# Optimization experiments

Hardware: AMD Instinct MI355X
Metric: run time of the kernel (lower is better)

Reference implementation:

```python
import jax, jax.numpy as jnp
import numpy as np
import math

N_HEAD = 16
D_MODEL = 1024
KSIZE = 3
PAD = 1


def _conv1d(x, w, b, pad):
    # x: [B, C_in, S], w: [C_out, C_in, K] (torch Conv1d layout)
    y = jax.lax.conv_general_dilated(
        x, w, window_strides=(1,), padding=[(pad, pad)],
        dimension_numbers=("NCH", "OIH", "NCH"))
    return y + b[None, :, None]


def setup_inputs() -> dict:
    key = jax.random.key(0)
    ks = jax.random.split(key, 10)
    B, S, D = 2, 2048, D_MODEL
    sc = 1.0 / math.sqrt(D)
    return {
        "q": jax.random.normal(ks[0], (B, S, D), jnp.float32),
        "k": jax.random.normal(ks[1], (B, S, D), jnp.float32),
        "v": jax.random.normal(ks[2], (B, S, D), jnp.float32),
        "wq_w": jax.random.normal(ks[3], (D, D, KSIZE), jnp.float32) * sc,
        "wq_b": jnp.zeros((D,), jnp.float32),
        "wk_w": jax.random.normal(ks[4], (D, D, KSIZE), jnp.float32) * sc,
        "wk_b": jnp.zeros((D,), jnp.float32),
        "wv_w": jax.random.normal(ks[5], (D, D, 1), jnp.float32) * sc,
        "wv_b": jnp.zeros((D,), jnp.float32),
        "wc_w": jax.random.normal(ks[6], (D, D), jnp.float32) * sc,
        "wc_b": jnp.zeros((D,), jnp.float32),
    }


def reference(q, k, v, wq_w, wq_b, wk_w, wk_b, wv_w, wv_b, wc_w, wc_b):
    B, S, D = q.shape
    h = N_HEAD
    d = D // h
    # channels-first for conv projections: [B, D, S]
    qc = _conv1d(jnp.swapaxes(q, 1, 2), wq_w, wq_b, PAD)
    kc = _conv1d(jnp.swapaxes(k, 1, 2), wk_w, wk_b, PAD)
    vc = _conv1d(jnp.swapaxes(v, 1, 2), wv_w, wv_b, 0)
    # faithful to torch: view(b, d, h, s) then transpose(1,2).transpose(2,3) -> [b, h, s, d]
    # (head index is the FAST axis of the channel dim, matching the original)
    qh = jnp.transpose(qc.reshape(B, d, h, S), (0, 2, 3, 1))
    kh = jnp.transpose(kc.reshape(B, d, h, S), (0, 2, 3, 1))
    vh = jnp.transpose(vc.reshape(B, d, h, S), (0, 2, 3, 1))
    scores = jnp.einsum("bhqd,bhkd->bhqk", qh, kh) / math.sqrt(d)
    attn = jax.nn.softmax(scores, axis=-1)
    out = jnp.einsum("bhqk,bhkd->bhqd", attn, vh)
    # concat: [b,h,s,d] -> [b,s,h*d]
    out = jnp.transpose(out, (0, 2, 1, 3)).reshape(B, S, D)
    # torch Linear: x @ W^T + b
    return out @ wc_w.T + wc_b
```

## Files before the change

kernel.cpp:

```cpp
#include <hip/hip_runtime.h>
#include <hip/hip_bf16.h>

#define SS 2048
#define DDIM 1024

typedef unsigned short u16;
typedef unsigned int u32;
typedef __attribute__((ext_vector_type(8))) short bf16x8_t;
typedef __attribute__((ext_vector_type(4))) float f32x4_t;

__device__ __forceinline__ u16 f2bf(float f) {
  __hip_bfloat16 h = __float2bfloat16(f);
  return *reinterpret_cast<u16*>(&h);
}

__device__ __forceinline__ void gld16(const void* g, void* lds_base) {
  __builtin_amdgcn_global_load_lds(
      (const __attribute__((address_space(1))) u32*)(uintptr_t)g,
      (__attribute__((address_space(3))) u32*)(u32)(uintptr_t)lds_base,
      16, 0, 0);
}

__global__ __launch_bounds__(256) void prep_kernel(
    const float* __restrict__ q, const float* __restrict__ k,
    const float* __restrict__ v, const float* __restrict__ wq_w,
    const float* __restrict__ wk_w, const float* __restrict__ wv_w,
    const float* __restrict__ wc_w, u16* __restrict__ Xq,
    u16* __restrict__ Xk, u16* __restrict__ Xv, u16* __restrict__ Wqr,
    u16* __restrict__ Wkr, u16* __restrict__ Wvr, u16* __restrict__ Wcr,
    u32* __restrict__ zbuf) {
  const int bid = blockIdx.x;
  const int tid = threadIdx.x;
  if (bid == 0 && tid < 64) zbuf[tid] = 0u;

  if (bid < 6144) {
    const int z = bid >> 11;
    const int bx = bid & 2047;
    const float* src = (z == 0) ? q : (z == 1) ? k : v;
    u16* dst = (z == 0) ? Xq : (z == 1) ? Xk : Xv;
    int i = bx * 256 + tid;
    const float4* s = (const float4*)src + (size_t)i * 2;
    float4 f0 = s[0], f1 = s[1];
    u16 o[8] = {f2bf(f0.x), f2bf(f0.y), f2bf(f0.z), f2bf(f0.w),
                f2bf(f1.x), f2bf(f1.y), f2bf(f1.z), f2bf(f1.w)};
    *(uint4*)(dst + (size_t)i * 8) = *(const uint4*)o;
  } else if (bid < 8192) {
    const int idx = bid - 6144;
    const float* w = (idx >= 1024) ? wk_w : wq_w;
    u16* out = (idx >= 1024) ? Wkr : Wqr;
    const int o = idx & 1023;
    for (int j = tid; j < 3072; j += 256) {
      int i = j / 3, t = j - i * 3;
      out[(size_t)o * 3072 + t * 1024 + i] = f2bf(w[(size_t)o * 3072 + j]);
    }
  } else {
    const int idx = bid - 8192;
    const float* w = (idx >= 1024) ? wc_w : wv_w;
    u16* out = (idx >= 1024) ? Wcr : Wvr;
    const int bx = idx & 1023;
    size_t i = (size_t)bx * 1024 + tid * 4;
    float4 f = *(const float4*)(w + i);
    u16 o4[4] = {f2bf(f.x), f2bf(f.y), f2bf(f.z), f2bf(f.w)};
    *(ushort4*)(out + i) = *(const ushort4*)o4;
  }
}

__global__ __launch_bounds__(256) void mfma_proj(
    const u16* __restrict__ Xq, const u16* __restrict__ Xk,
    const u16* __restrict__ Xv, const u16* __restrict__ Wq,
    const u16* __restrict__ Wk, const u16* __restrict__ Wv,
    const float* __restrict__ bq, const float* __restrict__ bk,
    const float* __restrict__ bv, u16* __restrict__ Qhb,
    u16* __restrict__ Khb, u16* __restrict__ Vtb,
    const u16* __restrict__ zbuf) {
  __shared__ __attribute__((aligned(16))) u16 As2[2][128][40];
  __shared__ __attribute__((aligned(16))) u16 Bs2[2][128][40];
  const int z = blockIdx.z;
  const u16* __restrict__ Xb = (z == 0) ? Xq : (z == 1) ? Xk : Xv;
  const u16* __restrict__ Wr = (z == 0) ? Wq : (z == 1) ? Wk : Wv;
  const float* __restrict__ bias = (z == 0) ? bq : (z == 1) ? bk : bv;
  u16* __restrict__ Cptr = (z == 0) ? Qhb : (z == 1) ? Khb : Vtb;
  const int nk = (z == 2) ? 32 : 96;
  const bool conv = (z < 2);
  const bool vout = (z == 2);
  const float scale = (z == 0) ? 0.125f : 1.0f;
  const int Kdim = (z == 2) ? 1024 : 3072;

  const int tid = threadIdx.x;
  const int lane = tid & 63;
  const int w = tid >> 6;
  const int ln = tid & 15;
  const int quad = (tid >> 4) & 3;
  const int wrow = w >> 1, wcol = w & 1;
  const int m0 = blockIdx.x * 128, n0 = blockIdx.y * 128;

  const char* p[5];
  int dinc[5];
  u32 ldso[5];
  bool act[5], isA[5], loA[5], hiA[5];
  const char* pbaseA[5];

#pragma unroll
  for (int i = 0; i < 5; ++i) {
    int c = w + 4 * i;
    isA[i] = (c < 10);
    if (c < 10) {
      int G = c * 64 + lane;
      int x = G / 5, kb = G - x * 5;
      int gm = m0 + x;
      int b = gm >> 11, s = gm & 2047;
      act[i] = (kb < 4);
      ldso[i] = c * 1024;
      const char* pb = (const char*)(Xb + (size_t)(b * SS + s) * DDIM + kb * 8);
      pbaseA[i] = pb;
      loA[i] = (s == 0);
      hiA[i] = (s == 2047);
      if (conv) {
        p[i] = loA[i] ? (const char*)zbuf : (pb - 2048);
        dinc[i] = loA[i] ? 0 : 64;
      } else {
        p[i] = pb;
        dinc[i] = 64;
      }
    } else {
      int c2 = c - 10;
      int G = c2 * 64 + lane;
      int x = G / 5, kb = G - x * 5;
      act[i] = (kb < 4);
      ldso[i] = c2 * 1024;
      p[i] = (const char*)(Wr + (size_t)(n0 + x) * Kdim + kb * 8);
      dinc[i] = 64;
      pbaseA[i] = nullptr;
      loA[i] = hiA[i] = false;
    }
  }

  auto stage = [&](int bi) {
#pragma unroll
    for (int i = 0; i < 5; ++i) {
      char* dst = (isA[i] ? (char*)As2[bi] : (char*)Bs2[bi]) + ldso[i];
      if (act[i]) gld16(p[i], dst);
      p[i] += dinc[i];
    }
  };

  f32x4_t acc[4][4];
#pragma unroll
  for (int i = 0; i < 4; ++i)
#pragma unroll
    for (int j = 0; j < 4; ++j) acc[i][j] = (f32x4_t){0.f, 0.f, 0.f, 0.f};

  stage(0);
  stage(1);

#pragma unroll 2
  for (int ks = 0; ks < nk; ++ks) {
    const int cur = ks & 1;
    if (ks + 1 < nk)
      asm volatile("s_waitcnt vmcnt(5)\ns_barrier" ::: "memory");
    else
      asm volatile("s_waitcnt vmcnt(0)\ns_barrier" ::: "memory");

    const u16(*As)[40] = As2[cur];
    const u16(*Bs)[40] = Bs2[cur];
    bf16x8_t a[4], b[4];
#pragma unroll
    for (int mt = 0; mt < 4; ++mt)
      a[mt] = *(const bf16x8_t*)&As[wrow * 64 + mt * 16 + ln][quad * 8];
#pragma unroll
    for (int nt = 0; nt < 4; ++nt)
      b[nt] = *(const bf16x8_t*)&Bs[wcol * 64 + nt * 16 + ln][quad * 8];
    __builtin_amdgcn_s_setprio(1);
#pragma unroll
    for (int mt = 0; mt < 4; ++mt)
#pragma unroll
      for (int nt = 0; nt < 4; ++nt)
        acc[mt][nt] = __builtin_amdgcn_mfma_f32_16x16x32_bf16(
            a[mt], b[nt], acc[mt][nt], 0, 0, 0);
    __builtin_amdgcn_s_setprio(0);

    asm volatile("s_waitcnt lgkmcnt(0)\ns_barrier" ::: "memory");
    __builtin_amdgcn_sched_barrier(0);

    const int j = ks + 2;
    if (j < nk) {
      if (conv && (j & 31) == 0) {
#pragma unroll
        for (int i = 0; i < 5; ++i) {
          if (isA[i]) {
            if (j == 32) {
              if (loA[i]) { p[i] = pbaseA[i]; dinc[i] = 64; }
            } else {
              if (hiA[i]) { p[i] = (const char*)zbuf; dinc[i] = 0; }
            }
          }
        }
      }
      stage(cur);
    }
  }

#pragma unroll
  for (int mt = 0; mt < 4; ++mt) {
#pragma unroll
    for (int nt = 0; nt < 4; ++nt) {
      int gn = n0 + wcol * 64 + nt * 16 + ln;
      float bi = bias[gn];
#pragma unroll
      for (int r = 0; r < 4; ++r) {
        int gm = m0 + wrow * 64 + mt * 16 + quad * 4 + r;
        float val = (acc[mt][nt][r] + bi) * scale;
        int b = gm >> 11, s = gm & 2047;
        int hh = gn & 15, dd = gn >> 4;
        if (!vout)
          Cptr[((size_t)(b * 16 + hh) * SS + s) * 64 + dd] = f2bf(val);
        else
          Cptr[((size_t)(b * 16 + hh) * 64 + dd) * SS + s] = f2bf(val);
      }
    }
  }
}

__global__ __launch_bounds__(256) void mfma_gemm_lin(
    const u16* __restrict__ Xb, const u16* __restrict__ Wr,
    const float* __restrict__ bias, float* __restrict__ Cptr) {
  __shared__ __attribute__((aligned(16))) u16 As2[2][32][40];
  __shared__ __attribute__((aligned(16))) u16 Bs2[2][128][40];
  const int tid = threadIdx.x;
  const int lane = tid & 63;
  const int w = tid >> 6;
  const int ln = tid & 15;
  const int quad = (tid >> 4) & 3;
  const int wrow = w >> 1, wcol = w & 1;
  const int m0 = blockIdx.x * 32, n0 = blockIdx.y * 128;

  const char* p[4];
  u32 ldso[4];
  bool ok[4], act[4], isA[4];
#pragma unroll
  for (int i = 0; i < 4; ++i) {
    int c = w + 4 * i;
    ok[i] = (c < 13);
    if (c < 3) {
      int G = c * 64 + lane;
      int x = G / 5, kb = G - x * 5;
      isA[i] = true;
      act[i] = (kb < 4) && (x < 32);
      ldso[i] = c * 1024;
      p[i] = (const char*)(Xb + (size_t)(m0 + x) * DDIM + kb * 8);
    } else if (c < 13) {
      int c2 = c - 3;
      int G = c2 * 64 + lane;
      int x = G / 5, kb = G - x * 5;
      isA[i] = false;
      act[i] = (kb < 4);
      ldso[i] = c2 * 1024;
      p[i] = (const char*)(Wr + (size_t)(n0 + x) * 1024 + kb * 8);
    } else {
      isA[i] = false; act[i] = false; ldso[i] = 0; p[i] = nullptr;
    }
  }

  auto stage = [&](int bi) {
#pragma unroll
    for (int i = 0; i < 4; ++i) {
      if (ok[i]) {
        char* dst = (isA[i] ? (char*)As2[bi] : (char*)Bs2[bi]) + ldso[i];
        if (act[i]) gld16(p[i], dst);
        p[i] += 64;
      }
    }
  };

  f32x4_t acc[4];
#pragma unroll
  for (int j = 0; j < 4; ++j) acc[j] = (f32x4_t){0.f, 0.f, 0.f, 0.f};

  stage(0);
  stage(1);

#pragma unroll 2
  for (int ks = 0; ks < 32; ++ks) {
    const int cur = ks & 1;
    if (ks + 1 < 32) {
      if (w == 0) asm volatile("s_waitcnt vmcnt(4)\ns_barrier" ::: "memory");
      else        asm volatile("s_waitcnt vmcnt(3)\ns_barrier" ::: "memory");
    } else {
      asm volatile("s_waitcnt vmcnt(0)\ns_barrier" ::: "memory");
    }

    const u16(*As)[40] = As2[cur];
    const u16(*Bs)[40] = Bs2[cur];
    bf16x8_t a = *(const bf16x8_t*)&As[wrow * 16 + ln][quad * 8];
    bf16x8_t b[4];
#pragma unroll
    for (int nt = 0; nt < 4; ++nt)
      b[nt] = *(const bf16x8_t*)&Bs[wcol * 64 + nt * 16 + ln][quad * 8];
    __builtin_amdgcn_s_setprio(1);
#pragma unroll
    for (int nt = 0; nt < 4; ++nt)
      acc[nt] = __builtin_amdgcn_mfma_f32_16x16x32_bf16(a, b[nt], acc[nt], 0, 0, 0);
    __builtin_amdgcn_s_setprio(0);

    asm volatile("s_waitcnt lgkmcnt(0)\ns_barrier" ::: "memory");
    __builtin_amdgcn_sched_barrier(0);

    if (ks + 2 < 32) stage(cur);
  }

#pragma unroll
  for (int nt = 0; nt < 4; ++nt) {
    int gn = n0 + wcol * 64 + nt * 16 + ln;
    float bi = bias[gn];
#pragma unroll
    for (int r = 0; r < 4; ++r) {
      int gm = m0 + wrow * 16 + quad * 4 + r;
      Cptr[(size_t)gm * DDIM + gn] = acc[nt][r] + bi;
    }
  }
}

__global__ __launch_bounds__(256) void mfma_attn(
    const u16* __restrict__ Qhb, const u16* __restrict__ Khb,
    const u16* __restrict__ Vtb, u16* __restrict__ Aob,
    const u16* __restrict__ zbuf) {
  __shared__ __attribute__((aligned(16))) u16 Ks2[2][64][72];
  __shared__ __attribute__((aligned(16))) u16 Vt2[2][64][72];
  __shared__ __attribute__((aligned(16))) u16 Ps[4][16][72];
  const int tid = threadIdx.x;
  const int lane = tid & 63;
  const int w = tid >> 6;
  const int ln = tid & 15;
  const int quad = (tid >> 4) & 3;
  const int bh = blockIdx.y;
  const int b = bh >> 4, hh = bh & 15;
  const int s0 = blockIdx.x * 64;

  const char* p[5];
  int dinc[5];
  u32 ldso[5];
  bool ok[5], act[5], isK[5];
#pragma unroll
  for (int i = 0; i < 5; ++i) {
    int c = w + 4 * i;
    ok[i] = (c < 18);
    if (c < 9) {
      int G = c * 64 + lane;
      int x = G / 9, db = G - x * 9;
      isK[i] = true;
      act[i] = (db < 8);
      ldso[i] = c * 1024;
      p[i] = (const char*)(Khb + ((size_t)bh * SS + x) * 64 + db * 8);
      dinc[i] = 8192;
    } else if (c < 18) {
      int c2 = c - 9;
      int G = c2 * 64 + lane;
      int x = G / 9, db = G - x * 9;
      isK[i] = false;
      act[i] = (db < 8);
      ldso[i] = c2 * 1024;
      p[i] = (const char*)(Vtb + ((size_t)bh * 64 + x) * SS + db * 8);
      dinc[i] = 128;
    } else {
      isK[i] = false; ok[i] = false; act[i] = false; ldso[i] = 0;
      p[i] = nullptr; dinc[i] = 0;
    }
  }

  auto stage = [&](int bi) {
#pragma unroll
    for (int i = 0; i < 5; ++i) {
      if (ok[i]) {
        char* dst = (isK[i] ? (char*)Ks2[bi] : (char*)Vt2[bi]) + ldso[i];
        if (act[i]) gld16(p[i], dst);
        p[i] += dinc[i];
      }
    }
  };

  const u16* qp = Qhb + ((size_t)bh * SS + s0 + w * 16 + ln) * 64 + quad * 8;
  bf16x8_t qf0 = *(const bf16x8_t*)qp;
  bf16x8_t qf1 = *(const bf16x8_t*)(qp + 32);

  float mrow = -3e38f;
  float lsum[4];
  f32x4_t oacc[4];
#pragma unroll
  for (int r = 0; r < 4; ++r) lsum[r] = 0.f;
#pragma unroll
  for (int dt = 0; dt < 4; ++dt) oacc[dt] = (f32x4_t){0.f, 0.f, 0.f, 0.f};

  stage(0);
  stage(1);

#pragma unroll 2
  for (int kt = 0; kt < 32; ++kt) {
    const int cur = kt & 1;
    if (kt + 1 < 32) {
      if (w < 2) asm volatile("s_waitcnt vmcnt(5)\ns_barrier" ::: "memory");
      else       asm volatile("s_waitcnt vmcnt(4)\ns_barrier" ::: "memory");
    } else {
      asm volatile("s_waitcnt vmcnt(0)\ns_barrier" ::: "memory");
    }

    const u16(*Ks)[72] = Ks2[cur];
    const u16(*Vt)[72] = Vt2[cur];

    f32x4_t sc[4];
#pragma unroll
    for (int nt = 0; nt < 4; ++nt) sc[nt] = (f32x4_t){0.f, 0.f, 0.f, 0.f};
    __builtin_amdgcn_s_setprio(1);
#pragma unroll
    for (int nt = 0; nt < 4; ++nt) {
      bf16x8_t k0f = *(const bf16x8_t*)&Ks[nt * 16 + ln][quad * 8];
      sc[nt] = __builtin_amdgcn_mfma_f32_16x16x32_bf16(qf0, k0f, sc[nt], 0, 0, 0);
      bf16x8_t k1f = *(const bf16x8_t*)&Ks[nt * 16 + ln][32 + quad * 8];
      sc[nt] = __builtin_amdgcn_mfma_f32_16x16x32_bf16(qf1, k1f, sc[nt], 0, 0, 0);
    }
    __builtin_amdgcn_s_setprio(0);

    float mx = sc[0][0];
#pragma unroll
    for (int nt = 0; nt < 4; ++nt)
#pragma unroll
      for (int r = 0; r < 4; ++r) mx = fmaxf(mx, sc[nt][r]);
    mx = fmaxf(mx, __shfl_xor(mx, 1, 64));
    mx = fmaxf(mx, __shfl_xor(mx, 2, 64));
    mx = fmaxf(mx, __shfl_xor(mx, 4, 64));
    mx = fmaxf(mx, __shfl_xor(mx, 8, 64));
    mx = fmaxf(mx, __shfl_xor(mx, 16, 64));
    mx = fmaxf(mx, __shfl_xor(mx, 32, 64));
    if (mx > mrow) {
      float al = __expf(mrow - mx);
      mrow = mx;
#pragma unroll
      for (int r = 0; r < 4; ++r) lsum[r] *= al;
#pragma unroll
      for (int dt = 0; dt < 4; ++dt)
#pragma unroll
        for (int r = 0; r < 4; ++r) oacc[dt][r] *= al;
    }
#pragma unroll
    for (int r = 0; r < 4; ++r) {
      float p0 = __expf(sc[0][r] - mrow), p1 = __expf(sc[1][r] - mrow);
      float p2 = __expf(sc[2][r] - mrow), p3 = __expf(sc[3][r] - mrow);
      lsum[r] += p0 + p1 + p2 + p3;
      Ps[w][quad * 4 + r][ln] = f2bf(p0);
      Ps[w][quad * 4 + r][16 + ln] = f2bf(p1);
      Ps[w][quad * 4 + r][32 + ln] = f2bf(p2);
      Ps[w][quad * 4 + r][48 + ln] = f2bf(p3);
    }

    bf16x8_t pa0 = *(const bf16x8_t*)&Ps[w][ln][quad * 8];
    bf16x8_t pa1 = *(const bf16x8_t*)&Ps[w][ln][32 + quad * 8];
    __builtin_amdgcn_s_setprio(1);
#pragma unroll
    for (int dt = 0; dt < 4; ++dt) {
      bf16x8_t v0f = *(const bf16x8_t*)&Vt[dt * 16 + ln][quad * 8];
      oacc[dt] = __builtin_amdgcn_mfma_f32_16x16x32_bf16(pa0, v0f, oacc[dt], 0, 0, 0);
      bf16x8_t v1f = *(const bf16x8_t*)&Vt[dt * 16 + ln][32 + quad * 8];
      oacc[dt] = __builtin_amdgcn_mfma_f32_16x16x32_bf16(pa1, v1f, oacc[dt], 0, 0, 0);
    }
    __builtin_amdgcn_s_setprio(0);

    asm volatile("s_waitcnt lgkmcnt(0)\ns_barrier" ::: "memory");
    __builtin_amdgcn_sched_barrier(0);
    if (kt + 2 < 32) stage(cur);
  }

  float inv[4];
#pragma unroll
  for (int r = 0; r < 4; ++r) {
    float t = lsum[r];
    t += __shfl_xor(t, 1, 64);
    t += __shfl_xor(t, 2, 64);
    t += __shfl_xor(t, 4, 64);
    t += __shfl_xor(t, 8, 64);
    inv[r] = 1.f / t;
  }
#pragma unroll
  for (int dt = 0; dt < 4; ++dt)
#pragma unroll
    for (int r = 0; r < 4; ++r) {
      int gm = b * SS + s0 + w * 16 + quad * 4 + r;
      Aob[(size_t)gm * DDIM + hh * 64 + dt * 16 + ln] = f2bf(oacc[dt][r] * inv[r]);
    }
}

extern "C" void kernel_launch(void* const* d_in, const int* in_sizes, int n_in,
                              void* d_out, int out_size, void* d_ws, size_t ws_size,
                              hipStream_t stream) {
  const float* q    = (const float*)d_in[0];
  const float* k    = (const float*)d_in[1];
  const float* v    = (const float*)d_in[2];
  const float* wq_w = (const float*)d_in[3];
  const float* wq_b = (const float*)d_in[4];
  const float* wk_w = (const float*)d_in[5];
  const float* wk_b = (const float*)d_in[6];
  const float* wv_w = (const float*)d_in[7];
  const float* wv_b = (const float*)d_in[8];
  const float* wc_w = (const float*)d_in[9];
  const float* wc_b = (const float*)d_in[10];

  char* ws = (char*)d_ws;
  size_t off = 0;
  u16* zbuf = (u16*)(ws + off); off += 256;
  const size_t SZ_ACT = (size_t)2 * SS * DDIM * 2;
  u16* Xq  = (u16*)(ws + off); off += SZ_ACT;
  u16* Xk  = (u16*)(ws + off); off += SZ_ACT;
  u16* Xv  = (u16*)(ws + off); off += SZ_ACT;
  u16* Wqr = (u16*)(ws + off); off += (size_t)1024 * 3072 * 2;
  u16* Wkr = (u16*)(ws + off); off += (size_t)1024 * 3072 * 2;
  u16* Wvr = (u16*)(ws + off); off += (size_t)1024 * 1024 * 2;
  u16* Wcr = (u16*)(ws + off); off += (size_t)1024 * 1024 * 2;
  u16* Qhb = (u16*)(ws + off); off += SZ_ACT;
  u16* Khb = (u16*)(ws + off); off += SZ_ACT;
  u16* Vtb = (u16*)(ws + off); off += SZ_ACT;
  u16* Aob = (u16*)(ws + off); off += SZ_ACT;
  if (ws_size < off) return;

  prep_kernel<<<10240, 256, 0, stream>>>(q, k, v, wq_w, wk_w, wv_w, wc_w,
                                         Xq, Xk, Xv, Wqr, Wkr, Wvr, Wcr,
                                         (u32*)zbuf);

  mfma_proj<<<dim3(32, 8, 3), 256, 0, stream>>>(
      Xq, Xk, Xv, Wqr, Wkr, Wvr, wq_b, wk_b, wv_b, Qhb, Khb, Vtb, zbuf);

  mfma_attn<<<dim3(32, 32), 256, 0, stream>>>(Qhb, Khb, Vtb, Aob, zbuf);

  mfma_gemm_lin<<<dim3(128, 8), 256, 0, stream>>>(Aob, Wcr, wc_b, (float*)d_out);
}
```

Baseline: 366.1 us.

## Triple-buffer LDS staging in all GEMM/attention kernels and fold log2e into Q scale

Moves the projection, output linear, and attention kernels from double to triple buffering of LDS tiles. Each of them now has two loads in flight while computing, with adjusted vmcnt waits and a rotating buffer index. Separately, the Q scale absorbs log2(e) so the softmax can use the native exp2 instruction instead of __expf. The extra LDS per block may lower occupancy, and the rotating index in place of the unroll-by-2 parity adds some scalar overhead.

```diff
diff --git a/kernel.cpp b/kernel.cpp
--- a/kernel.cpp
+++ b/kernel.cpp
@@ -72,9 +72,9 @@
     const float* __restrict__ bq, const float* __restrict__ bk,
     const float* __restrict__ bv, u16* __restrict__ Qhb,
     u16* __restrict__ Khb, u16* __restrict__ Vtb,
-    const u16* __restrict__ zbuf) {
-  __shared__ __attribute__((aligned(16))) u16 As2[2][128][40];
-  __shared__ __attribute__((aligned(16))) u16 Bs2[2][128][40];
+    const u16* __restrict__ zbuf, float qscale) {
+  __shared__ __attribute__((aligned(16))) u16 As3[3][128][40];
+  __shared__ __attribute__((aligned(16))) u16 Bs3[3][128][40];
   const int z = blockIdx.z;
   const u16* __restrict__ Xb = (z == 0) ? Xq : (z == 1) ? Xk : Xv;
   const u16* __restrict__ Wr = (z == 0) ? Wq : (z == 1) ? Wk : Wv;
@@ -83,7 +83,7 @@
   const int nk = (z == 2) ? 32 : 96;
   const bool conv = (z < 2);
   const bool vout = (z == 2);
-  const float scale = (z == 0) ? 0.125f : 1.0f;
+  const float scale = (z == 0) ? qscale : 1.0f;
   const int Kdim = (z == 2) ? 1024 : 3072;
 
   const int tid = threadIdx.x;
@@ -104,6 +104,8 @@
   for (int i = 0; i < 5; ++i) {
     int c = w + 4 * i;
     isA[i] = (c < 10);
+    loA[i] = hiA[i] = false;
+    pbaseA[i] = nullptr;
     if (c < 10) {
       int G = c * 64 + lane;
       int x = G / 5, kb = G - x * 5;
@@ -130,15 +132,13 @@
       ldso[i] = c2 * 1024;
       p[i] = (const char*)(Wr + (size_t)(n0 + x) * Kdim + kb * 8);
       dinc[i] = 64;
-      pbaseA[i] = nullptr;
-      loA[i] = hiA[i] = false;
     }
   }
 
   auto stage = [&](int bi) {
 #pragma unroll
     for (int i = 0; i < 5; ++i) {
-      char* dst = (isA[i] ? (char*)As2[bi] : (char*)Bs2[bi]) + ldso[i];
+      char* dst = (isA[i] ? (char*)As3[bi] : (char*)Bs3[bi]) + ldso[i];
       if (act[i]) gld16(p[i], dst);
       p[i] += dinc[i];
     }
@@ -152,17 +152,17 @@
 
   stage(0);
   stage(1);
-
-#pragma unroll 2
+  stage(2);
+
+  int cur = 0;
   for (int ks = 0; ks < nk; ++ks) {
-    const int cur = ks & 1;
-    if (ks + 1 < nk)
-      asm volatile("s_waitcnt vmcnt(5)\ns_barrier" ::: "memory");
-    else
-      asm volatile("s_waitcnt vmcnt(0)\ns_barrier" ::: "memory");
-
-    const u16(*As)[40] = As2[cur];
-    const u16(*Bs)[40] = Bs2[cur];
+    const int rem = nk - ks;
+    if (rem >= 3)      asm volatile("s_waitcnt vmcnt(10)\ns_barrier" ::: "memory");
+    else if (rem == 2) asm volatile("s_waitcnt vmcnt(5)\ns_barrier" ::: "memory");
+    else               asm volatile("s_waitcnt vmcnt(0)\ns_barrier" ::: "memory");
+
+    const u16(*As)[40] = As3[cur];
+    const u16(*Bs)[40] = Bs3[cur];
     bf16x8_t a[4], b[4];
 #pragma unroll
     for (int mt = 0; mt < 4; ++mt)
@@ -182,7 +182,7 @@
     asm volatile("s_waitcnt lgkmcnt(0)\ns_barrier" ::: "memory");
     __builtin_amdgcn_sched_barrier(0);
 
-    const int j = ks + 2;
+    const int j = ks + 3;
     if (j < nk) {
       if (conv && (j & 31) == 0) {
 #pragma unroll
@@ -198,6 +198,7 @@
       }
       stage(cur);
     }
+    cur = (cur == 2) ? 0 : cur + 1;
   }
 
 #pragma unroll
@@ -224,8 +225,8 @@
 __global__ __launch_bounds__(256) void mfma_gemm_lin(
     const u16* __restrict__ Xb, const u16* __restrict__ Wr,
     const float* __restrict__ bias, float* __restrict__ Cptr) {
-  __shared__ __attribute__((aligned(16))) u16 As2[2][32][40];
-  __shared__ __attribute__((aligned(16))) u16 Bs2[2][128][40];
+  __shared__ __attribute__((aligned(16))) u16 As3[3][32][40];
+  __shared__ __attribute__((aligned(16))) u16 Bs3[3][128][40];
   const int tid = threadIdx.x;
   const int lane = tid & 63;
   const int w = tid >> 6;
@@ -265,7 +266,7 @@
 #pragma unroll
     for (int i = 0; i < 4; ++i) {
       if (ok[i]) {
-        char* dst = (isA[i] ? (char*)As2[bi] : (char*)Bs2[bi]) + ldso[i];
+        char* dst = (isA[i] ? (char*)As3[bi] : (char*)Bs3[bi]) + ldso[i];
         if (act[i]) gld16(p[i], dst);
         p[i] += 64;
       }
@@ -278,19 +279,23 @@
 
   stage(0);
   stage(1);
-
-#pragma unroll 2
+  stage(2);
+
+  int cur = 0;
   for (int ks = 0; ks < 32; ++ks) {
-    const int cur = ks & 1;
-    if (ks + 1 < 32) {
+    const int rem = 32 - ks;
+    if (rem >= 3) {
+      if (w == 0) asm volatile("s_waitcnt vmcnt(8)\ns_barrier" ::: "memory");
+      else        asm volatile("s_waitcnt vmcnt(6)\ns_barrier" ::: "memory");
+    } else if (rem == 2) {
       if (w == 0) asm volatile("s_waitcnt vmcnt(4)\ns_barrier" ::: "memory");
       else        asm volatile("s_waitcnt vmcnt(3)\ns_barrier" ::: "memory");
     } else {
       asm volatile("s_waitcnt vmcnt(0)\ns_barrier" ::: "memory");
     }
 
-    const u16(*As)[40] = As2[cur];
-    const u16(*Bs)[40] = Bs2[cur];
+    const u16(*As)[40] = As3[cur];
+    const u16(*Bs)[40] = Bs3[cur];
     bf16x8_t a = *(const bf16x8_t*)&As[wrow * 16 + ln][quad * 8];
     bf16x8_t b[4];
 #pragma unroll
@@ -305,7 +310,8 @@
     asm volatile("s_waitcnt lgkmcnt(0)\ns_barrier" ::: "memory");
     __builtin_amdgcn_sched_barrier(0);
 
-    if (ks + 2 < 32) stage(cur);
+    if (ks + 3 < 32) stage(cur);
+    cur = (cur == 2) ? 0 : cur + 1;
   }
 
 #pragma unroll
@@ -324,8 +330,8 @@
     const u16* __restrict__ Qhb, const u16* __restrict__ Khb,
     const u16* __restrict__ Vtb, u16* __restrict__ Aob,
     const u16* __restrict__ zbuf) {
-  __shared__ __attribute__((aligned(16))) u16 Ks2[2][64][72];
-  __shared__ __attribute__((aligned(16))) u16 Vt2[2][64][72];
+  __shared__ __attribute__((aligned(16))) u16 Ks3[3][64][72];
+  __shared__ __attribute__((aligned(16))) u16 Vt3[3][64][72];
   __shared__ __attribute__((aligned(16))) u16 Ps[4][16][72];
   const int tid = threadIdx.x;
   const int lane = tid & 63;
@@ -371,7 +377,7 @@
 #pragma unroll
     for (int i = 0; i < 5; ++i) {
       if (ok[i]) {
-        char* dst = (isK[i] ? (char*)Ks2[bi] : (char*)Vt2[bi]) + ldso[i];
+        char* dst = (isK[i] ? (char*)Ks3[bi] : (char*)Vt3[bi]) + ldso[i];
         if (act[i]) gld16(p[i], dst);
         p[i] += dinc[i];
       }
@@ -392,19 +398,23 @@
 
   stage(0);
   stage(1);
-
-#pragma unroll 2
+  stage(2);
+
+  int cur = 0;
   for (int kt = 0; kt < 32; ++kt) {
-    const int cur = kt & 1;
-    if (kt + 1 < 32) {
+    const int rem = 32 - kt;
+    if (rem >= 3) {
+      if (w < 2) asm volatile("s_waitcnt vmcnt(10)\ns_barrier" ::: "memory");
+      else       asm volatile("s_waitcnt vmcnt(8)\ns_barrier" ::: "memory");
+    } else if (rem == 2) {
       if (w < 2) asm volatile("s_waitcnt vmcnt(5)\ns_barrier" ::: "memory");
       else       asm volatile("s_waitcnt vmcnt(4)\ns_barrier" ::: "memory");
     } else {
       asm volatile("s_waitcnt vmcnt(0)\ns_barrier" ::: "memory");
     }
 
-    const u16(*Ks)[72] = Ks2[cur];
-    const u16(*Vt)[72] = Vt2[cur];
+    const u16(*Ks)[72] = Ks3[cur];
+    const u16(*Vt)[72] = Vt3[cur];
 
     f32x4_t sc[4];
 #pragma unroll
@@ -431,7 +441,7 @@
     mx = fmaxf(mx, __shfl_xor(mx, 16, 64));
     mx = fmaxf(mx, __shfl_xor(mx, 32, 64));
     if (mx > mrow) {
-      float al = __expf(mrow - mx);
+      float al = __builtin_amdgcn_exp2f(mrow - mx);
       mrow = mx;
 #pragma unroll
       for (int r = 0; r < 4; ++r) lsum[r] *= al;
@@ -442,8 +452,10 @@
     }
 #pragma unroll
     for (int r = 0; r < 4; ++r) {
-      float p0 = __expf(sc[0][r] - mrow), p1 = __expf(sc[1][r] - mrow);
-      float p2 = __expf(sc[2][r] - mrow), p3 = __expf(sc[3][r] - mrow);
+      float p0 = __builtin_amdgcn_exp2f(sc[0][r] - mrow);
+      float p1 = __builtin_amdgcn_exp2f(sc[1][r] - mrow);
+      float p2 = __builtin_amdgcn_exp2f(sc[2][r] - mrow);
+      float p3 = __builtin_amdgcn_exp2f(sc[3][r] - mrow);
       lsum[r] += p0 + p1 + p2 + p3;
       Ps[w][quad * 4 + r][ln] = f2bf(p0);
       Ps[w][quad * 4 + r][16 + ln] = f2bf(p1);
@@ -465,7 +477,8 @@
 
     asm volatile("s_waitcnt lgkmcnt(0)\ns_barrier" ::: "memory");
     __builtin_amdgcn_sched_barrier(0);
-    if (kt + 2 < 32) stage(cur);
+    if (kt + 3 < 32) stage(cur);
+    cur = (cur == 2) ? 0 : cur + 1;
   }
 
   float inv[4];
@@ -524,7 +537,8 @@
                                          (u32*)zbuf);
 
   mfma_proj<<<dim3(32, 8, 3), 256, 0, stream>>>(
-      Xq, Xk, Xv, Wqr, Wkr, Wvr, wq_b, wk_b, wv_b, Qhb, Khb, Vtb, zbuf);
+      Xq, Xk, Xv, Wqr, Wkr, Wvr, wq_b, wk_b, wv_b, Qhb, Khb, Vtb, zbuf,
+      0.125f * 1.44269504f);
 
   mfma_attn<<<dim3(32, 32), 256, 0, stream>>>(Qhb, Khb, Vtb, Aob, zbuf);
 
```

Result: slower. 379.2 us (+3.6%).
